# Performance work log

Measured on AMD Instinct MI355X. Metric: run time of the kernel, lower is better.

## Reference

```python
import jax, jax.numpy as jnp
import numpy as np

B, S1, S2, D1, D2 = 4, 2048, 2048, 512, 512
H, DK, DV = 8, 64, 64


def setup_inputs() -> dict:
    key = jax.random.key(0)
    ks = jax.random.split(key, 8)
    x1 = jax.random.normal(ks[0], (B, S1, D1), dtype=jnp.float32)
    x2 = jax.random.normal(ks[1], (B, S2, D2), dtype=jnp.float32)
    x3 = jax.random.normal(ks[2], (B, S2, D2), dtype=jnp.float32)
    s = 0.02
    Wq = jax.random.normal(ks[3], (D1, H * DK), dtype=jnp.float32) * s
    Wk = jax.random.normal(ks[4], (D2, H * DK), dtype=jnp.float32) * s
    Wv = jax.random.normal(ks[5], (D2, H * DV), dtype=jnp.float32) * s
    Wo = jax.random.normal(ks[6], (H * DV, D1), dtype=jnp.float32) * s
    bo = jnp.zeros((D1,), dtype=jnp.float32)
    return {"x1": x1, "x2": x2, "x3": x3, "Wq": Wq, "Wk": Wk, "Wv": Wv, "Wo": Wo, "bo": bo}


def reference(x1, x2, x3, Wq, Wk, Wv, Wo, bo):
    b, s1, _ = x1.shape
    # project to per-head q, k, v: [B, H, S, Dh]
    q = (x1 @ Wq).reshape(b, s1, H, DK).transpose(0, 2, 1, 3)
    k = (x2 @ Wk).reshape(b, x2.shape[1], H, DK).transpose(0, 2, 1, 3)
    v = (x3 @ Wv).reshape(b, x3.shape[1], H, DV).transpose(0, 2, 1, 3)
    scores = jnp.einsum('bhqd,bhkd->bhqk', q, k) / jnp.sqrt(jnp.float32(DK))
    attn = jax.nn.softmax(scores, axis=-1)
    out = jnp.einsum('bhqk,bhkd->bhqd', attn, v)  # [B, H, S1, DV]
    out = out.transpose(0, 2, 1, 3).reshape(b, s1, H * DV)
    return out @ Wo + bo
```

## Files before the change

kernel.cpp:

```cpp
#include <hip/hip_runtime.h>

typedef __attribute__((ext_vector_type(4))) float f32x4;
typedef __attribute__((ext_vector_type(8))) __bf16 bf16x8;
typedef __attribute__((ext_vector_type(4))) __bf16 bf16x4;

#define DEVINL __device__ __forceinline__

DEVINL void gld16(const void* g, void* l) {
  __builtin_amdgcn_global_load_lds((__attribute__((address_space(1))) void*)(void*)g,
                                   (__attribute__((address_space(3))) void*)l, 16, 0, 0);
}


__global__ __launch_bounds__(256) void cvt_all(const float* x1, const float* x2, const float* x3,
                                               const float* Wq, const float* Wk, const float* Wv,
                                               const float* Wo, __bf16* o0, __bf16* o1, __bf16* o2,
                                               __bf16* WT) {
  __shared__ float t[64][65];
  const int bx = blockIdx.x;
  if (bx < 12288) {
    const int z = bx >> 12;
    const float* s = z == 0 ? x1 : z == 1 ? x2 : x3;
    __bf16* d = z == 0 ? o0 : z == 1 ? o1 : o2;
    size_t i = (size_t)(bx & 4095) * 256 + threadIdx.x;
    f32x4 v = ((const f32x4*)s)[i];
    bf16x4 o;
#pragma unroll
    for (int j = 0; j < 4; ++j) o[j] = (__bf16)v[j];
    ((bf16x4*)d)[i] = o;
  } else {
    const int l = bx - 12288;
    const int z = l >> 6;
    const float* W = z == 0 ? Wq : z == 1 ? Wk : z == 2 ? Wv : Wo;
    __bf16* D = WT + (size_t)z * 512 * 512;
    const int r0 = ((l >> 3) & 7) * 64, c0 = (l & 7) * 64;
    const int tx = threadIdx.x & 63, ty = threadIdx.x >> 6;
#pragma unroll
    for (int j = 0; j < 16; ++j)
      t[ty + j * 4][tx] = W[(size_t)(r0 + ty + j * 4) * 512 + c0 + tx];
    __syncthreads();
#pragma unroll
    for (int j = 0; j < 16; ++j)
      D[(size_t)(c0 + ty + j * 4) * 512 + r0 + tx] = (__bf16)t[tx][ty + j * 4];
  }
}


DEVINL void gemm_tile(const __bf16* A, const __bf16* Bt, int m0, int n0,
                      __bf16* As, __bf16* Bs, f32x4 acc[4][4]) {
  const int tid = threadIdx.x, lane = tid & 63, w = tid >> 6;
  const int qd = lane >> 4, r = lane & 15;
  const int wm = w & 1, wn = w >> 1;
  const char* ap[4];
  const char* bp[4];
#pragma unroll
  for (int j = 0; j < 4; ++j) {
    int c = (w * 4 + j) * 64 + lane;
    int row = c >> 3, cs = c & 7;
    int gc = cs ^ (row & 7);
    ap[j] = (const char*)A + (size_t)(m0 + row) * 1024 + gc * 16;
    bp[j] = (const char*)Bt + (size_t)(n0 + row) * 1024 + gc * 16;
  }
  int offA[4][2], offB[4][2];
#pragma unroll
  for (int t = 0; t < 4; ++t)
#pragma unroll
    for (int ks = 0; ks < 2; ++ks) {
      int m = wm * 64 + t * 16 + r;
      offA[t][ks] = m * 128 + (((ks * 4 + qd) ^ (m & 7)) * 16);
      int n = wn * 64 + t * 16 + r;
      offB[t][ks] = n * 128 + (((ks * 4 + qd) ^ (n & 7)) * 16);
    }
  char* AsC = (char*)As;
  char* BsC = (char*)Bs;
  for (int kt = 0; kt < 8; ++kt) {
    __syncthreads();
#pragma unroll
    for (int j = 0; j < 4; ++j) {
      gld16(ap[j] + kt * 128, AsC + (w * 4 + j) * 1024);
      gld16(bp[j] + kt * 128, BsC + (w * 4 + j) * 1024);
    }
    __syncthreads();
#pragma unroll
    for (int ks = 0; ks < 2; ++ks) {
      bf16x8 a[4], b[4];
#pragma unroll
      for (int t = 0; t < 4; ++t) {
        a[t] = *(const bf16x8*)(AsC + offA[t][ks]);
        b[t] = *(const bf16x8*)(BsC + offB[t][ks]);
      }
#pragma unroll
      for (int i = 0; i < 4; ++i)
#pragma unroll
        for (int j2 = 0; j2 < 4; ++j2)
          acc[i][j2] = __builtin_amdgcn_mfma_f32_16x16x32_bf16(a[i], b[j2], acc[i][j2], 0, 0, 0);
    }
  }
}

__global__ __launch_bounds__(256, 3) void gemm_proj(const __bf16* x1b, const __bf16* x2b,
                                                    const __bf16* x3b, const __bf16* WT,
                                                    __bf16* Qo, __bf16* Ko, __bf16* Vto) {
  __shared__ __align__(16) char smem[34816];
  __bf16* As = (__bf16*)smem;
  __bf16* Bs = (__bf16*)(smem + 16384);
  const int z = blockIdx.z;
  const __bf16* A = z == 0 ? x1b : z == 1 ? x2b : x3b;
  const __bf16* Bt = WT + (size_t)z * 512 * 512;
  const int l = blockIdx.x;
  const int sidx = l >> 3;
  const int m0 = ((l & 7) * 8 + (sidx >> 2)) * 128;
  const int n0 = (sidx & 3) * 128;
  f32x4 acc[4][4] = {};
  gemm_tile(A, Bt, m0, n0, As, Bs, acc);
  const int tid = threadIdx.x, lane = tid & 63, w = tid >> 6;
  const int qd = lane >> 4, r = lane & 15, wm = w & 1, wn = w >> 1;
  const int b = m0 >> 11, sbase = m0 & 2047;
  if (z == 2) {
    __syncthreads();
    char* T = smem;
#pragma unroll
    for (int mt = 0; mt < 4; ++mt)
#pragma unroll
      for (int nt = 0; nt < 4; ++nt) {
        int dv = wn * 64 + nt * 16 + r;
        int sl = wm * 64 + mt * 16 + qd * 4;
        bf16x4 p4;
#pragma unroll
        for (int g = 0; g < 4; ++g) p4[g] = (__bf16)acc[mt][nt][g];
        *(bf16x4*)(T + (size_t)dv * 272 + sl * 2) = p4;
      }
    __syncthreads();
#pragma unroll
    for (int p2 = 0; p2 < 2; ++p2) {
      int dvrow = p2 * 64 + (tid >> 2);
      int col = n0 + dvrow, h = col >> 6, d = col & 63;
      __bf16* dst = Vto + ((size_t)(b * 8 + h) * 64 + d) * 2048 + sbase + (tid & 3) * 8;
#pragma unroll
      for (int j = 0; j < 4; ++j) {
        bf16x8 vv = *(const bf16x8*)(T + (size_t)dvrow * 272 + (tid & 3) * 16 + j * 64);
        *(bf16x8*)(dst + j * 32) = vv;
      }
    }
  } else {
    const float qscale = 0.18033688f;
#pragma unroll
    for (int mt = 0; mt < 4; ++mt) {
#pragma unroll
      for (int nt = 0; nt < 4; ++nt) {
        f32x4 v = acc[mt][nt];
        if (z == 0) {
#pragma unroll
          for (int g = 0; g < 4; ++g) v[g] *= qscale;
        }
        int col = n0 + wn * 64 + nt * 16 + r;
        int h = col >> 6, d = col & 63;
        int s = sbase + wm * 64 + mt * 16 + qd * 4;
        __bf16* O = (z == 0 ? Qo : Ko) + ((size_t)(b * 8 + h) * 2048 + s) * 64 + d;
#pragma unroll
        for (int g = 0; g < 4; ++g) O[(size_t)g * 64] = (__bf16)v[g];
      }
    }
  }
}

__global__ __launch_bounds__(256, 2) void gemm_out(const __bf16* Op, const float* Lp,
                                                   const __bf16* WoT, const float* bo,
                                                   float* out) {
  __shared__ __align__(16) __bf16 As[64 * 64];
  __shared__ __align__(16) __bf16 Bs[128 * 64];
  const int tid = threadIdx.x, lane = tid & 63, w = tid >> 6;
  const int qd = lane >> 4, r = lane & 15, wm = w & 1, wn = w >> 1;
  const int id = blockIdx.x;
  const int rest = id >> 3;
  const int m0 = ((id & 7) * 16 + (rest & 15)) * 64;
  const int n0 = (rest >> 4) * 128;
  const int b8 = (m0 >> 11) * 8;
  const int sb = m0 & 2047;
  const char* bp[4];
#pragma unroll
  for (int j = 0; j < 4; ++j) {
    int c = (w * 4 + j) * 64 + lane;
    int row = c >> 3, gc = (c & 7) ^ (row & 7);
    bp[j] = (const char*)WoT + (size_t)(n0 + row) * 1024 + gc * 16;
  }
  int arow[2], ach[2];
#pragma unroll
  for (int j = 0; j < 2; ++j) {
    int c = (w * 2 + j) * 64 + lane;
    arow[j] = c >> 3;
    ach[j] = c & 7;
  }
  int offA[2][2], offB[4][2];
#pragma unroll
  for (int ks = 0; ks < 2; ++ks) {
#pragma unroll
    for (int t = 0; t < 2; ++t) {
      int m = wm * 32 + t * 16 + r;
      offA[t][ks] = m * 128 + (((ks * 4 + qd) ^ (m & 7)) * 16);
    }
#pragma unroll
    for (int t = 0; t < 4; ++t) {
      int n = wn * 64 + t * 16 + r;
      offB[t][ks] = n * 128 + (((ks * 4 + qd) ^ (n & 7)) * 16);
    }
  }
  char* AsC = (char*)As;
  char* BsC = (char*)Bs;
  bf16x8 pa0[2], pa1[2];
  float pinv[2];
  auto loadA = [&](int h) {
#pragma unroll
    for (int j = 0; j < 2; ++j) {
      size_t rr = (size_t)(b8 + h) * 2048 + sb + arow[j];
      const __bf16* p0 = Op + rr * 64 + ach[j] * 8;
      pa0[j] = *(const bf16x8*)p0;
      pa1[j] = *(const bf16x8*)(p0 + (size_t)32 * 2048 * 64);
      pinv[j] = 1.0f / (Lp[rr] + Lp[rr + 65536]);
    }
  };
  loadA(0);
  f32x4 acc[2][4] = {};
  for (int kt = 0; kt < 8; ++kt) {
    __syncthreads();
#pragma unroll
    for (int j = 0; j < 4; ++j) gld16(bp[j] + kt * 128, BsC + (w * 4 + j) * 1024);
#pragma unroll
    for (int j = 0; j < 2; ++j) {
      bf16x8 q;
#pragma unroll
      for (int k2 = 0; k2 < 8; ++k2)
        q[k2] = (__bf16)(((float)pa0[j][k2] + (float)pa1[j][k2]) * pinv[j]);
      *(bf16x8*)(AsC + arow[j] * 128 + (ach[j] ^ (arow[j] & 7)) * 16) = q;
    }
    __syncthreads();
    if (kt < 7) loadA(kt + 1);
#pragma unroll
    for (int ks = 0; ks < 2; ++ks) {
      bf16x8 a[2], b[4];
#pragma unroll
      for (int t = 0; t < 2; ++t) a[t] = *(const bf16x8*)(AsC + offA[t][ks]);
#pragma unroll
      for (int t = 0; t < 4; ++t) b[t] = *(const bf16x8*)(BsC + offB[t][ks]);
#pragma unroll
      for (int i = 0; i < 2; ++i)
#pragma unroll
        for (int j2 = 0; j2 < 4; ++j2)
          acc[i][j2] = __builtin_amdgcn_mfma_f32_16x16x32_bf16(a[i], b[j2], acc[i][j2], 0, 0, 0);
    }
  }
#pragma unroll
  for (int nt = 0; nt < 4; ++nt) {
    int col = n0 + wn * 64 + nt * 16 + r;
    float bv = bo[col];
#pragma unroll
    for (int mt = 0; mt < 2; ++mt) {
      int mg = m0 + wm * 32 + mt * 16 + qd * 4;
#pragma unroll
      for (int g = 0; g < 4; ++g) out[(size_t)(mg + g) * 512 + col] = acc[mt][nt][g] + bv;
    }
  }
}

__global__ __launch_bounds__(256, 4) void attn(const __bf16* Q, const __bf16* K,
                                               const __bf16* Vt, __bf16* Opart, float* Lp) {
  __shared__ __align__(16) __bf16 QPs[128 * 64];
  __shared__ __align__(16) __bf16 Ksd[2][64 * 64];
  __shared__ __align__(16) __bf16 Vs[64 * 64];
  const int tid = threadIdx.x, lane = tid & 63, w = tid >> 6;
  const int qd = lane >> 4, r = lane & 15;
  const int id = blockIdx.x;
  const int rest = id >> 3;
  const int bh = (id & 7) * 4 + (rest >> 5);
  const int kvh = (rest >> 4) & 1;
  const int q0 = (rest & 15) * 128;
  const __bf16* Qg = Q + ((size_t)bh * 2048 + q0) * 64;
  const __bf16* Kg = K + (size_t)bh * 2048 * 64;
  const __bf16* Vg = Vt + (size_t)bh * 64 * 2048;
  char* PsC = (char*)QPs;
  char* Ks0 = (char*)Ksd;
  char* Ks1 = (char*)Ksd + 8192;
  char* VsC = (char*)Vs;

  const char* Kst[2];
  const char* Vst[2];
  int ldso[2];
#pragma unroll
  for (int j = 0; j < 2; ++j) {
    int c = (w * 2 + j) * 64 + lane;
    int m = c >> 3, gc = (c & 7) ^ (m & 7);
    Kst[j] = (const char*)Kg + (size_t)m * 128 + gc * 16;
    Vst[j] = (const char*)Vg + (size_t)m * 4096 + gc * 16;
    ldso[j] = (w * 2 + j) * 1024;
  }

  const int kt0 = kvh * 16;

#pragma unroll
  for (int j = 0; j < 4; ++j) {
    int c = (w * 4 + j) * 64 + lane;
    int m = c >> 3, gc = (c & 7) ^ (m & 7);
    gld16((const char*)Qg + m * 128 + gc * 16, PsC + (w * 4 + j) * 1024);
  }
#pragma unroll
  for (int j = 0; j < 2; ++j) gld16(Kst[j] + (size_t)kt0 * 8192, Ks0 + ldso[j]);
  asm volatile("s_waitcnt vmcnt(0)" ::: "memory");
  __builtin_amdgcn_sched_barrier(0);
  __builtin_amdgcn_s_barrier();
  __builtin_amdgcn_sched_barrier(0);

  bf16x8 qf[2][2];
#pragma unroll
  for (int mt = 0; mt < 2; ++mt)
#pragma unroll
    for (int ks = 0; ks < 2; ++ks) {
      int m = w * 32 + mt * 16 + r;
      qf[mt][ks] = *(const bf16x8*)(PsC + m * 128 + ((ks * 4 + qd) ^ (m & 7)) * 16);
    }

  int offKV[4][2];
#pragma unroll
  for (int t = 0; t < 4; ++t)
#pragma unroll
    for (int ks = 0; ks < 2; ++ks) {
      int n = t * 16 + r;
      offKV[t][ks] = n * 128 + ((ks * 4 + qd) ^ (n & 7)) * 16;
    }

  bf16x8 ones;
#pragma unroll
  for (int j = 0; j < 8; ++j) ones[j] = (__bf16)1.0f;
  const f32x4 z4 = {};

  f32x4 oacc[2][4] = {};
  f32x4 lacc[2] = {};

  auto iter = [&](int kt, int ktn, char* Kc, char* Kn) {
    gld16(Vst[0] + (size_t)kt * 128, VsC + ldso[0]);
    gld16(Vst[1] + (size_t)kt * 128, VsC + ldso[1]);
    gld16(Kst[0] + (size_t)ktn * 8192, Kn + ldso[0]);
    gld16(Kst[1] + (size_t)ktn * 8192, Kn + ldso[1]);
    __builtin_amdgcn_sched_barrier(0);

    f32x4 sf[2][4];
    __builtin_amdgcn_s_setprio(1);
#pragma unroll
    for (int nt = 0; nt < 4; ++nt) {
      bf16x8 kf0 = *(const bf16x8*)(Kc + offKV[nt][0]);
      bf16x8 kf1 = *(const bf16x8*)(Kc + offKV[nt][1]);
#pragma unroll
      for (int mt = 0; mt < 2; ++mt) {
        f32x4 t0 = __builtin_amdgcn_mfma_f32_16x16x32_bf16(kf0, qf[mt][0], z4, 0, 0, 0);
        sf[mt][nt] = __builtin_amdgcn_mfma_f32_16x16x32_bf16(kf1, qf[mt][1], t0, 0, 0, 0);
      }
    }
    __builtin_amdgcn_s_setprio(0);
#pragma unroll
    for (int mt = 0; mt < 2; ++mt) {
      int q = w * 32 + mt * 16 + r;
#pragma unroll
      for (int nt = 0; nt < 4; ++nt) {
        bf16x4 p4;
#pragma unroll
        for (int g = 0; g < 4; ++g) p4[g] = (__bf16)__builtin_exp2f(sf[mt][nt][g]);
        *(bf16x4*)(PsC + q * 128 + (((2 * nt + (qd >> 1)) ^ (q & 7)) * 16) + (qd & 1) * 8) = p4;
      }
    }

    asm volatile("s_waitcnt vmcnt(2)" ::: "memory");
    __builtin_amdgcn_sched_barrier(0);
    __builtin_amdgcn_s_barrier();
    __builtin_amdgcn_sched_barrier(0);

    __builtin_amdgcn_s_setprio(1);
#pragma unroll
    for (int mt = 0; mt < 2; ++mt) {
      int q = w * 32 + mt * 16 + r;
      bf16x8 pf0 = *(const bf16x8*)(PsC + q * 128 + ((qd ^ (q & 7)) * 16));
      bf16x8 pf1 = *(const bf16x8*)(PsC + q * 128 + (((4 + qd) ^ (q & 7)) * 16));
      lacc[mt] = __builtin_amdgcn_mfma_f32_16x16x32_bf16(pf0, ones, lacc[mt], 0, 0, 0);
      lacc[mt] = __builtin_amdgcn_mfma_f32_16x16x32_bf16(pf1, ones, lacc[mt], 0, 0, 0);
#pragma unroll
      for (int dvt = 0; dvt < 4; ++dvt) {
        bf16x8 vf0 = *(const bf16x8*)(VsC + offKV[dvt][0]);
        bf16x8 vf1 = *(const bf16x8*)(VsC + offKV[dvt][1]);
        oacc[mt][dvt] = __builtin_amdgcn_mfma_f32_16x16x32_bf16(pf0, vf0, oacc[mt][dvt], 0, 0, 0);
        oacc[mt][dvt] = __builtin_amdgcn_mfma_f32_16x16x32_bf16(pf1, vf1, oacc[mt][dvt], 0, 0, 0);
      }
    }
    __builtin_amdgcn_s_setprio(0);

    asm volatile("s_waitcnt vmcnt(0)" ::: "memory");
    __builtin_amdgcn_sched_barrier(0);
    __builtin_amdgcn_s_barrier();
    __builtin_amdgcn_sched_barrier(0);
  };

#pragma unroll 1
  for (int kt = kt0; kt < kt0 + 16; kt += 2) {
    iter(kt, kt + 1, Ks0, Ks1);
    int kt2 = (kt + 2 < kt0 + 16) ? kt + 2 : kt + 1;
    iter(kt + 1, kt2, Ks1, Ks0);
  }

  const size_t pbase = (size_t)(kvh * 32 + bh) * 2048;
#pragma unroll
  for (int mt = 0; mt < 2; ++mt) {
    if (r == 0) {
#pragma unroll
      for (int g = 0; g < 4; ++g)
        Lp[pbase + q0 + w * 32 + mt * 16 + qd * 4 + g] = lacc[mt][g];
    }
  }
  __bf16* Ob0 = Opart + pbase * 64;
#pragma unroll
  for (int mt = 0; mt < 2; ++mt) {
#pragma unroll
    for (int g = 0; g < 4; ++g) {
      int s = q0 + w * 32 + mt * 16 + qd * 4 + g;
#pragma unroll
      for (int dvt = 0; dvt < 4; ++dvt)
        Ob0[(size_t)s * 64 + dvt * 16 + r] = (__bf16)oacc[mt][dvt][g];
    }
  }
}


extern "C" void kernel_launch(void* const* d_in, const int* in_sizes, int n_in,
                              void* d_out, int out_size, void* d_ws, size_t ws_size,
                              hipStream_t stream) {
  const float* x1 = (const float*)d_in[0];
  const float* x2 = (const float*)d_in[1];
  const float* x3 = (const float*)d_in[2];
  const float* Wq = (const float*)d_in[3];
  const float* Wk = (const float*)d_in[4];
  const float* Wv = (const float*)d_in[5];
  const float* Wo = (const float*)d_in[6];
  const float* bo = (const float*)d_in[7];
  float* out = (float*)d_out;
  char* ws = (char*)d_ws;
  const size_t MB = 1ull << 20;
  __bf16* x1b = (__bf16*)(ws);
  __bf16* x2b = (__bf16*)(ws + 8 * MB);
  __bf16* x3b = (__bf16*)(ws + 16 * MB);
  __bf16* WT = (__bf16*)(ws + 24 * MB);
  __bf16* Qb = (__bf16*)(ws + 26 * MB);
  __bf16* Kb = (__bf16*)(ws + 34 * MB);
  __bf16* Vtb = (__bf16*)(ws + 42 * MB);
  __bf16* Opart = (__bf16*)(ws + 58 * MB);
  float* Lp = (float*)(ws + 74 * MB);

  cvt_all<<<dim3(12544), 256, 0, stream>>>(x1, x2, x3, Wq, Wk, Wv, Wo, x1b, x2b, x3b, WT);
  gemm_proj<<<dim3(256, 1, 3), 256, 0, stream>>>(x1b, x2b, x3b, WT, Qb, Kb, Vtb);
  attn<<<dim3(1024), 256, 0, stream>>>(Qb, Kb, Vtb, Opart, Lp);
  gemm_out<<<dim3(512), 256, 0, stream>>>(Opart, Lp, WT + 3ull * 512 * 512, bo, out);
}
```

Measured before the change: 191.1 us.

## Switch attention to 32x32x16 MFMA and keep P in registers

The attention kernel moves from 16x16x32 MFMA tiles to 32x32x16 tiles, so each wave computes S^T = K·Q^T for its 32 queries in two 32-key blocks. The K load permutes rows so that the accumulator layout of exp(S) lines up with the A-operand layout of the P·V MFMA. P is packed straight from registers into bf16x8 fragments instead of being written to and read back from LDS. This removes the LDS round trip for P and lowers the MFMA instruction count, at the cost of larger accumulators (f32x16) and more register pressure under the 4-blocks-per-CU launch bound.

```diff
diff --git a/kernel.cpp b/kernel.cpp
--- a/kernel.cpp
+++ b/kernel.cpp
@@ -1,8 +1,11 @@
 #include <hip/hip_runtime.h>
 
 typedef __attribute__((ext_vector_type(4))) float f32x4;
+typedef __attribute__((ext_vector_type(16))) float f32x16;
 typedef __attribute__((ext_vector_type(8))) __bf16 bf16x8;
 typedef __attribute__((ext_vector_type(4))) __bf16 bf16x4;
+typedef __attribute__((ext_vector_type(2))) __bf16 bf16x2;
+typedef __attribute__((ext_vector_type(4))) unsigned u32x4;
 
 #define DEVINL __device__ __forceinline__
 
@@ -264,11 +267,11 @@
 
 __global__ __launch_bounds__(256, 4) void attn(const __bf16* Q, const __bf16* K,
                                                const __bf16* Vt, __bf16* Opart, float* Lp) {
-  __shared__ __align__(16) __bf16 QPs[128 * 64];
+  __shared__ __align__(16) __bf16 Qs[128 * 64];
   __shared__ __align__(16) __bf16 Ksd[2][64 * 64];
   __shared__ __align__(16) __bf16 Vs[64 * 64];
   const int tid = threadIdx.x, lane = tid & 63, w = tid >> 6;
-  const int qd = lane >> 4, r = lane & 15;
+  const int l31 = lane & 31, lh = lane >> 5;
   const int id = blockIdx.x;
   const int rest = id >> 3;
   const int bh = (id & 7) * 4 + (rest >> 5);
@@ -277,7 +280,7 @@
   const __bf16* Qg = Q + ((size_t)bh * 2048 + q0) * 64;
   const __bf16* Kg = K + (size_t)bh * 2048 * 64;
   const __bf16* Vg = Vt + (size_t)bh * 64 * 2048;
-  char* PsC = (char*)QPs;
+  char* QsC = (char*)Qs;
   char* Ks0 = (char*)Ksd;
   char* Ks1 = (char*)Ksd + 8192;
   char* VsC = (char*)Vs;
@@ -289,7 +292,8 @@
   for (int j = 0; j < 2; ++j) {
     int c = (w * 2 + j) * 64 + lane;
     int m = c >> 3, gc = (c & 7) ^ (m & 7);
-    Kst[j] = (const char*)Kg + (size_t)m * 128 + gc * 16;
+    int ms = (m & ~12) | ((m & 4) << 1) | ((m & 8) >> 1);
+    Kst[j] = (const char*)Kg + (size_t)ms * 128 + gc * 16;
     Vst[j] = (const char*)Vg + (size_t)m * 4096 + gc * 16;
     ldso[j] = (w * 2 + j) * 1024;
   }
@@ -300,7 +304,7 @@
   for (int j = 0; j < 4; ++j) {
     int c = (w * 4 + j) * 64 + lane;
     int m = c >> 3, gc = (c & 7) ^ (m & 7);
-    gld16((const char*)Qg + m * 128 + gc * 16, PsC + (w * 4 + j) * 1024);
+    gld16((const char*)Qg + m * 128 + gc * 16, QsC + (w * 4 + j) * 1024);
   }
 #pragma unroll
   for (int j = 0; j < 2; ++j) gld16(Kst[j] + (size_t)kt0 * 8192, Ks0 + ldso[j]);
@@ -309,31 +313,20 @@
   __builtin_amdgcn_s_barrier();
   __builtin_amdgcn_sched_barrier(0);
 
-  bf16x8 qf[2][2];
-#pragma unroll
-  for (int mt = 0; mt < 2; ++mt)
-#pragma unroll
-    for (int ks = 0; ks < 2; ++ks) {
-      int m = w * 32 + mt * 16 + r;
-      qf[mt][ks] = *(const bf16x8*)(PsC + m * 128 + ((ks * 4 + qd) ^ (m & 7)) * 16);
-    }
-
-  int offKV[4][2];
-#pragma unroll
-  for (int t = 0; t < 4; ++t)
-#pragma unroll
-    for (int ks = 0; ks < 2; ++ks) {
-      int n = t * 16 + r;
-      offKV[t][ks] = n * 128 + ((ks * 4 + qd) ^ (n & 7)) * 16;
-    }
+  const int rb = l31 * 128;
+  const int he = (((lane & 7) ^ lh) << 4);
+
+  bf16x8 qf[4];
+#pragma unroll
+  for (int c = 0; c < 4; ++c)
+    qf[c] = *(const bf16x8*)(QsC + (w * 32 + l31) * 128 + ((c << 5) ^ he));
 
   bf16x8 ones;
 #pragma unroll
   for (int j = 0; j < 8; ++j) ones[j] = (__bf16)1.0f;
-  const f32x4 z4 = {};
-
-  f32x4 oacc[2][4] = {};
-  f32x4 lacc[2] = {};
+
+  f32x16 oacc[2] = {};
+  f32x16 lacc = {};
 
   auto iter = [&](int kt, int ktn, char* Kc, char* Kn) {
     gld16(Vst[0] + (size_t)kt * 128, VsC + ldso[0]);
@@ -342,29 +335,31 @@
     gld16(Kst[1] + (size_t)ktn * 8192, Kn + ldso[1]);
     __builtin_amdgcn_sched_barrier(0);
 
-    f32x4 sf[2][4];
-    __builtin_amdgcn_s_setprio(1);
-#pragma unroll
-    for (int nt = 0; nt < 4; ++nt) {
-      bf16x8 kf0 = *(const bf16x8*)(Kc + offKV[nt][0]);
-      bf16x8 kf1 = *(const bf16x8*)(Kc + offKV[nt][1]);
-#pragma unroll
-      for (int mt = 0; mt < 2; ++mt) {
-        f32x4 t0 = __builtin_amdgcn_mfma_f32_16x16x32_bf16(kf0, qf[mt][0], z4, 0, 0, 0);
-        sf[mt][nt] = __builtin_amdgcn_mfma_f32_16x16x32_bf16(kf1, qf[mt][1], t0, 0, 0, 0);
-      }
-    }
-    __builtin_amdgcn_s_setprio(0);
-#pragma unroll
-    for (int mt = 0; mt < 2; ++mt) {
-      int q = w * 32 + mt * 16 + r;
-#pragma unroll
-      for (int nt = 0; nt < 4; ++nt) {
-        bf16x4 p4;
-#pragma unroll
-        for (int g = 0; g < 4; ++g) p4[g] = (__bf16)__builtin_exp2f(sf[mt][nt][g]);
-        *(bf16x4*)(PsC + q * 128 + (((2 * nt + (qd >> 1)) ^ (q & 7)) * 16) + (qd & 1) * 8) = p4;
-      }
+    unsigned pk[2][8];
+#pragma unroll
+    for (int t2 = 0; t2 < 2; ++t2) {
+      f32x16 s = {};
+      __builtin_amdgcn_s_setprio(1);
+#pragma unroll
+      for (int c = 0; c < 4; ++c) {
+        bf16x8 kf = *(const bf16x8*)(Kc + t2 * 4096 + rb + ((c << 5) ^ he));
+        s = __builtin_amdgcn_mfma_f32_32x32x16_bf16(kf, qf[c], s, 0, 0, 0);
+      }
+      __builtin_amdgcn_s_setprio(0);
+#pragma unroll
+      for (int i = 0; i < 8; ++i) {
+        bf16x2 t;
+        t[0] = (__bf16)__builtin_exp2f(s[2 * i]);
+        t[1] = (__bf16)__builtin_exp2f(s[2 * i + 1]);
+        pk[t2][i] = __builtin_bit_cast(unsigned, t);
+      }
+    }
+    bf16x8 pa[4];
+#pragma unroll
+    for (int c = 0; c < 4; ++c) {
+      u32x4 u = {pk[c >> 1][(c & 1) * 4 + 0], pk[c >> 1][(c & 1) * 4 + 1],
+                 pk[c >> 1][(c & 1) * 4 + 2], pk[c >> 1][(c & 1) * 4 + 3]};
+      pa[c] = __builtin_bit_cast(bf16x8, u);
     }
 
     asm volatile("s_waitcnt vmcnt(2)" ::: "memory");
@@ -374,18 +369,12 @@
 
     __builtin_amdgcn_s_setprio(1);
 #pragma unroll
-    for (int mt = 0; mt < 2; ++mt) {
-      int q = w * 32 + mt * 16 + r;
-      bf16x8 pf0 = *(const bf16x8*)(PsC + q * 128 + ((qd ^ (q & 7)) * 16));
-      bf16x8 pf1 = *(const bf16x8*)(PsC + q * 128 + (((4 + qd) ^ (q & 7)) * 16));
-      lacc[mt] = __builtin_amdgcn_mfma_f32_16x16x32_bf16(pf0, ones, lacc[mt], 0, 0, 0);
-      lacc[mt] = __builtin_amdgcn_mfma_f32_16x16x32_bf16(pf1, ones, lacc[mt], 0, 0, 0);
-#pragma unroll
-      for (int dvt = 0; dvt < 4; ++dvt) {
-        bf16x8 vf0 = *(const bf16x8*)(VsC + offKV[dvt][0]);
-        bf16x8 vf1 = *(const bf16x8*)(VsC + offKV[dvt][1]);
-        oacc[mt][dvt] = __builtin_amdgcn_mfma_f32_16x16x32_bf16(pf0, vf0, oacc[mt][dvt], 0, 0, 0);
-        oacc[mt][dvt] = __builtin_amdgcn_mfma_f32_16x16x32_bf16(pf1, vf1, oacc[mt][dvt], 0, 0, 0);
+    for (int c = 0; c < 4; ++c) {
+      lacc = __builtin_amdgcn_mfma_f32_32x32x16_bf16(pa[c], ones, lacc, 0, 0, 0);
+#pragma unroll
+      for (int dvt = 0; dvt < 2; ++dvt) {
+        bf16x8 vf = *(const bf16x8*)(VsC + dvt * 4096 + rb + ((c << 5) ^ he));
+        oacc[dvt] = __builtin_amdgcn_mfma_f32_32x32x16_bf16(pa[c], vf, oacc[dvt], 0, 0, 0);
       }
     }
     __builtin_amdgcn_s_setprio(0);
@@ -404,23 +393,18 @@
   }
 
   const size_t pbase = (size_t)(kvh * 32 + bh) * 2048;
-#pragma unroll
-  for (int mt = 0; mt < 2; ++mt) {
-    if (r == 0) {
-#pragma unroll
-      for (int g = 0; g < 4; ++g)
-        Lp[pbase + q0 + w * 32 + mt * 16 + qd * 4 + g] = lacc[mt][g];
-    }
+  if (l31 == 0) {
+#pragma unroll
+    for (int g = 0; g < 16; ++g)
+      Lp[pbase + q0 + w * 32 + (g & 3) + 8 * (g >> 2) + 4 * lh] = lacc[g];
   }
   __bf16* Ob0 = Opart + pbase * 64;
 #pragma unroll
-  for (int mt = 0; mt < 2; ++mt) {
-#pragma unroll
-    for (int g = 0; g < 4; ++g) {
-      int s = q0 + w * 32 + mt * 16 + qd * 4 + g;
-#pragma unroll
-      for (int dvt = 0; dvt < 4; ++dvt)
-        Ob0[(size_t)s * 64 + dvt * 16 + r] = (__bf16)oacc[mt][dvt][g];
+  for (int dvt = 0; dvt < 2; ++dvt) {
+#pragma unroll
+    for (int g = 0; g < 16; ++g) {
+      int s = q0 + w * 32 + (g & 3) + 8 * (g >> 2) + 4 * lh;
+      Ob0[(size_t)s * 64 + dvt * 32 + l31] = (__bf16)oacc[dvt][g];
     }
   }
 }
```

Measured after the change: 194.3 us. No clear change (+1.6%).
